# Kernel optimization log

Measured on AMD Instinct MI355X. Metric: run time of the kernel, lower is better.

## Reference

```python
import math
import jax, jax.numpy as jnp
from jax import lax
import numpy as np

LIDAR_MAX_X = 32.0
LIDAR_MAX_Y = 32.0
NQ = 1280  # eval-branch num_queries hardcoded in the torch module


def sineembed(pos, hidden_dim=256):
    # pos (..., 2) -> (..., hidden_dim); DAB-DETR sine embedding
    half = hidden_dim // 2
    dim_t = 10000.0 ** (2.0 * (jnp.arange(half) // 2).astype(jnp.float32) / half)
    scale = 2.0 * math.pi
    px = (pos[..., 0] * scale)[..., None] / dim_t
    py = (pos[..., 1] * scale)[..., None] / dim_t

    def interleave(p):
        s = jnp.stack([jnp.sin(p[..., 0::2]), jnp.cos(p[..., 1::2])], axis=-1)
        return s.reshape(s.shape[:-2] + (-1,))

    return jnp.concatenate([interleave(py), interleave(px)], axis=-1)


def grid_sample_bilinear_zeros(value, grid):
    # value (B,C,H,W); grid (B,Hg,Wg,2) in [-1,1], (x,y) order,
    # bilinear, padding_mode='zeros', align_corners=False
    B, C, H, W = value.shape
    Hg, Wg = grid.shape[1], grid.shape[2]
    gx = ((grid[..., 0] + 1.0) * 0.5 * W - 0.5).reshape(B, -1)
    gy = ((grid[..., 1] + 1.0) * 0.5 * H - 0.5).reshape(B, -1)
    x0 = jnp.floor(gx)
    y0 = jnp.floor(gy)
    wx1 = gx - x0
    wy1 = gy - y0
    vflat = value.reshape(B, C, H * W)

    def gather(ix, iy, w):
        valid = (ix >= 0) & (ix <= W - 1) & (iy >= 0) & (iy <= H - 1)
        ixc = jnp.clip(ix, 0, W - 1).astype(jnp.int32)
        iyc = jnp.clip(iy, 0, H - 1).astype(jnp.int32)
        idx = iyc * W + ixc  # (B,N)
        v = jnp.take_along_axis(vflat, idx[:, None, :], axis=2)  # (B,C,N)
        return v * (w * valid)[:, None, :]

    out = (gather(x0, y0, (1 - wx1) * (1 - wy1))
           + gather(x0 + 1, y0, wx1 * (1 - wy1))
           + gather(x0, y0 + 1, (1 - wx1) * wy1)
           + gather(x0 + 1, y0 + 1, wx1 * wy1))
    return out.reshape(B, C, Hg, Wg)


def setup_inputs() -> dict:
    key = jax.random.key(0)
    ks = jax.random.split(key, 12)
    B, D, Cin, H, W = 8, 256, 64, 200, 200
    return {
        "queries": jax.random.normal(ks[0], (B, NQ, D), jnp.float32),
        "navi_points": jax.random.normal(ks[1], (B, 2), jnp.float32) * 10.0,
        "bev_feature": jax.random.normal(ks[2], (B, Cin, H, W), jnp.float32),
        "spatial_shape": jnp.array([H, W], jnp.int32),
        "point_score": jax.random.uniform(ks[3], (B, 2), jnp.float32),
        "aw_w": jax.random.normal(ks[4], (1, D), jnp.float32) * 0.02,
        "aw_b": jnp.zeros((1,), jnp.float32),
        "aws_w": jax.random.normal(ks[5], (1, D), jnp.float32) * 0.02,
        "aws_b": jnp.zeros((1,), jnp.float32),
        "conv_w": jax.random.normal(ks[6], (256, Cin, 3, 3), jnp.float32) * 0.02,
        "conv_b": jnp.zeros((256,), jnp.float32),
        "out_w": jax.random.normal(ks[7], (D, D), jnp.float32) * 0.02,
        "out_b": jnp.zeros((D,), jnp.float32),
    }


def reference(queries, navi_points, bev_feature, spatial_shape, point_score,
              aw_w, aw_b, aws_w, aws_b, conv_w, conv_b, out_w, out_b):
    B, nq, D = queries.shape
    # eval branch: expand navi_points to (B, 1280, 1, 2)
    pts = jnp.broadcast_to(navi_points.reshape(B, 1, 1, 2), (B, NQ, 1, 2))
    # normalize then swap -> grid (x=pts_y/max_x, y=pts_x/max_y)
    grid = jnp.stack([pts[..., 1] / LIDAR_MAX_X, pts[..., 0] / LIDAR_MAX_Y], axis=-1)

    # attention weights from queries, softmax over num_points (=1)
    aw = jax.nn.softmax(queries @ aw_w.T + aw_b, axis=-1)  # (B,NQ,1)

    # score weights from sine embedding of point_score
    ps = jnp.broadcast_to(point_score.reshape(B, 1, 1, 2), (B, NQ, 1, 2))
    aws = (sineembed(ps) @ aws_w.T + aws_b).reshape(B, NQ, 1)  # (B,NQ,1)

    # value projection: Conv2d 64->256, 3x3, pad 1, ReLU
    value = lax.conv_general_dilated(bev_feature, conv_w, (1, 1), 'SAME',
                                     dimension_numbers=('NCHW', 'OIHW', 'NCHW'))
    value = jax.nn.relu(value + conv_b[None, :, None, None])

    sampled = grid_sample_bilinear_zeros(value, grid)  # (B,256,NQ,1)

    out = (aw[:, None] * sampled * aws[:, None]).sum(axis=-1)  # (B,256,NQ)
    out = out.transpose(0, 2, 1)  # (B,NQ,256)
    out = out @ out_w.T + out_b
    return out + queries  # dropout is identity at inference
```

## Files before the change

kernel.cpp:

```cpp
#include <hip/hip_runtime.h>
#include <math.h>

#define NQ   1280
#define DD   256
#define CIN  64
#define HH   200
#define WW   200
#define KW   576

__device__ __forceinline__ float wave_reduce(float v) {
#pragma unroll
    for (int off = 32; off > 0; off >>= 1) v += __shfl_down(v, off, 64);
    return v;
}

__global__ __launch_bounds__(256) void conv_sample_kernel(
    const float* __restrict__ navi,
    const float* __restrict__ bev,
    const float* __restrict__ pscore,
    const float* __restrict__ aws_w,
    const float* __restrict__ aws_b,
    const float* __restrict__ conv_w,
    const float* __restrict__ conv_b,
    float* __restrict__ s_out,
    float* __restrict__ aws_out)
{
    const int b    = blockIdx.x >> 6;
    const int cg   = blockIdx.x & 63;
    const int tid  = threadIdx.x;
    const int lane = tid & 63;
    const int wave = tid >> 6;

    __shared__ float win[CIN][16];
    __shared__ float wv[4][KW];
    __shared__ float red[DD];

    float nx = navi[b * 2 + 0];
    float ny = navi[b * 2 + 1];
    float gx = (ny * (1.0f / 32.0f) + 1.0f) * 0.5f * (float)WW - 0.5f;
    float gy = (nx * (1.0f / 32.0f) + 1.0f) * 0.5f * (float)HH - 0.5f;
    float x0f = floorf(gx), y0f = floorf(gy);
    float wx1 = gx - x0f, wy1 = gy - y0f;
    int x0 = (int)x0f, y0 = (int)y0f;

    float cw[4];
    {
        float wx[2] = {1.0f - wx1, wx1};
        float wy[2] = {1.0f - wy1, wy1};
#pragma unroll
        for (int k = 0; k < 4; ++k) {
            int dx = k & 1, dy = k >> 1;
            float ixf = x0f + (float)dx, iyf = y0f + (float)dy;
            bool valid = (ixf >= 0.0f) && (ixf <= (float)(WW - 1)) &&
                         (iyf >= 0.0f) && (iyf <= (float)(HH - 1));
            cw[k] = wx[dx] * wy[dy] * (valid ? 1.0f : 0.0f);
        }
    }

    for (int idx = tid; idx < CIN * 16; idx += 256) {
        int ci = idx >> 4, pos = idx & 15;
        int yy = y0 - 1 + (pos >> 2);
        int xx = x0 - 1 + (pos & 3);
        float v = 0.0f;
        if (yy >= 0 && yy < HH && xx >= 0 && xx < WW)
            v = bev[((size_t)b * CIN + ci) * (HH * WW) + (size_t)yy * WW + xx];
        win[ci][pos] = v;
    }
    __syncthreads();

    for (int idx = tid; idx < 4 * KW; idx += 256) {
        int corner = idx / KW, k = idx - corner * KW;
        int ci = k / 9, r = k - ci * 9;
        int ky = r / 3, kx = r - ky * 3;
        int dy = corner >> 1, dx = corner & 1;
        wv[corner][k] = win[ci][(ky + dy) * 4 + (kx + dx)];
    }
    __syncthreads();

    const int c = cg * 4 + wave;
    const float* wp = conv_w + (size_t)c * KW;
    float a0 = 0.f, a1 = 0.f, a2 = 0.f, a3 = 0.f;
#pragma unroll
    for (int i = 0; i < 9; ++i) {
        float w = wp[i * 64 + lane];
        a0 = fmaf(w, wv[0][i * 64 + lane], a0);
        a1 = fmaf(w, wv[1][i * 64 + lane], a1);
        a2 = fmaf(w, wv[2][i * 64 + lane], a2);
        a3 = fmaf(w, wv[3][i * 64 + lane], a3);
    }
    a0 = wave_reduce(a0);
    a1 = wave_reduce(a1);
    a2 = wave_reduce(a2);
    a3 = wave_reduce(a3);
    if (lane == 0) {
        float cb = conv_b[c];
        float v0 = fmaxf(a0 + cb, 0.0f);
        float v1 = fmaxf(a1 + cb, 0.0f);
        float v2 = fmaxf(a2 + cb, 0.0f);
        float v3 = fmaxf(a3 + cb, 0.0f);
        s_out[b * DD + c] = cw[0] * v0 + cw[1] * v1 + cw[2] * v2 + cw[3] * v3;
    }

    if (cg == 0) {
        float psx = pscore[b * 2 + 0];
        float psy = pscore[b * 2 + 1];
        float p = (tid < 128) ? psy : psx;
        int j = (tid & 127) >> 1;
        float dimt = powf(10000.0f, (float)j * (1.0f / 64.0f));
        float arg = p * 6.283185307179586f / dimt;
        float e = (tid & 1) ? cosf(arg) : sinf(arg);
        red[tid] = e * aws_w[tid];
        __syncthreads();
        for (int off = 128; off > 0; off >>= 1) {
            if (tid < off) red[tid] += red[tid + off];
            __syncthreads();
        }
        if (tid == 0) aws_out[b] = red[0] + aws_b[0];
    }
}

__global__ __launch_bounds__(256) void matvec_kernel(
    const float* __restrict__ out_w,
    const float* __restrict__ out_b,
    const float* __restrict__ s_in,
    const float* __restrict__ aws_in,
    float* __restrict__ t_out)
{
    const int b    = blockIdx.x >> 6;
    const int cg   = blockIdx.x & 63;
    const int tid  = threadIdx.x;
    const int lane = tid & 63;
    const int wave = tid >> 6;

    __shared__ float s_sh[DD];
    s_sh[tid] = s_in[b * DD + tid];
    __syncthreads();

    const int d = cg * 4 + wave;
    const float* wp = out_w + (size_t)d * DD;
    float sum = 0.0f;
#pragma unroll
    for (int i = 0; i < 4; ++i)
        sum = fmaf(wp[i * 64 + lane], s_sh[i * 64 + lane], sum);
    sum = wave_reduce(sum);
    if (lane == 0) t_out[b * DD + d] = aws_in[b] * sum + out_b[d];
}

__global__ __launch_bounds__(256) void add_kernel(
    const float4* __restrict__ q4,
    const float4* __restrict__ t4,
    float4* __restrict__ out4,
    int total4)
{
    int i = blockIdx.x * blockDim.x + threadIdx.x;
    if (i >= total4) return;
    float4 v = q4[i];
    int d4 = i & (DD / 4 - 1);
    int b = i / (NQ * DD / 4);
    float4 tv = t4[b * (DD / 4) + d4];
    v.x += tv.x; v.y += tv.y; v.z += tv.z; v.w += tv.w;
    out4[i] = v;
}

extern "C" void kernel_launch(void* const* d_in, const int* in_sizes, int n_in,
                              void* d_out, int out_size, void* d_ws, size_t ws_size,
                              hipStream_t stream) {
    const float* queries = (const float*)d_in[0];
    const float* navi    = (const float*)d_in[1];
    const float* bev     = (const float*)d_in[2];
    const float* pscore  = (const float*)d_in[4];
    const float* aws_w   = (const float*)d_in[7];
    const float* aws_b   = (const float*)d_in[8];
    const float* conv_w  = (const float*)d_in[9];
    const float* conv_b  = (const float*)d_in[10];
    const float* out_w   = (const float*)d_in[11];
    const float* out_b   = (const float*)d_in[12];
    float* out = (float*)d_out;

    const int B = in_sizes[1] / 2;

    float* s   = (float*)d_ws;
    float* aws = s + B * DD;
    float* t   = s + B * DD + 256;

    conv_sample_kernel<<<B * 64, 256, 0, stream>>>(navi, bev, pscore, aws_w,
                                                   aws_b, conv_w, conv_b, s, aws);
    matvec_kernel<<<B * 64, 256, 0, stream>>>(out_w, out_b, s, aws, t);

    int total4 = B * NQ * DD / 4;
    add_kernel<<<(total4 + 255) / 256, 256, 0, stream>>>(
        (const float4*)queries, (const float4*)t, (float4*)out, total4);
}
```

Measured before the change: 145.6 us.

## Fuse conv-sample, matvec and residual add into one cooperative kernel

Replaces three kernel launches with a single cooperative launch of 512 blocks that uses grid-wide syncs between the conv/sample stage, the output projection matvec, and the residual add. The conv stage now indexes the shared 4x4 window directly instead of building a per-corner staging buffer, which drops one shared-memory pass and a barrier. The residual add is done by a fixed grid that loops over the output. This aims to remove launch overhead and inter-kernel gaps, at the cost of grid.sync latency and a fixed batch size hardcoded at compile time.

```diff
diff --git a/kernel.cpp b/kernel.cpp
--- a/kernel.cpp
+++ b/kernel.cpp
@@ -1,12 +1,20 @@
 #include <hip/hip_runtime.h>
+#include <hip/hip_cooperative_groups.h>
 #include <math.h>
+
+namespace cg = cooperative_groups;
 
 #define NQ   1280
 #define DD   256
 #define CIN  64
 #define HH   200
 #define WW   200
+#define BB   8
 #define KW   576
+#define GRID 512
+#define TPB  256
+#define NTH  (GRID * TPB)
+#define TOTAL4 (BB * NQ * DD / 4)
 
 __device__ __forceinline__ float wave_reduce(float v) {
 #pragma unroll
@@ -14,7 +22,7 @@
     return v;
 }
 
-__global__ __launch_bounds__(256) void conv_sample_kernel(
+__global__ __launch_bounds__(256) void fused_kernel(
     const float* __restrict__ navi,
     const float* __restrict__ bev,
     const float* __restrict__ pscore,
@@ -22,144 +30,139 @@
     const float* __restrict__ aws_b,
     const float* __restrict__ conv_w,
     const float* __restrict__ conv_b,
-    float* __restrict__ s_out,
-    float* __restrict__ aws_out)
+    const float* __restrict__ out_w,
+    const float* __restrict__ out_b,
+    const float4* __restrict__ q4,
+    float4* __restrict__ out4,
+    float* __restrict__ s_g,
+    float* __restrict__ aws_g,
+    float* __restrict__ t_g)
 {
+    cg::grid_group grid = cg::this_grid();
     const int b    = blockIdx.x >> 6;
-    const int cg   = blockIdx.x & 63;
+    const int cgp  = blockIdx.x & 63;
     const int tid  = threadIdx.x;
     const int lane = tid & 63;
     const int wave = tid >> 6;
 
-    __shared__ float win[CIN][16];
-    __shared__ float wv[4][KW];
+    __shared__ float win[CIN * 16];
     __shared__ float red[DD];
 
-    float nx = navi[b * 2 + 0];
-    float ny = navi[b * 2 + 1];
-    float gx = (ny * (1.0f / 32.0f) + 1.0f) * 0.5f * (float)WW - 0.5f;
-    float gy = (nx * (1.0f / 32.0f) + 1.0f) * 0.5f * (float)HH - 0.5f;
-    float x0f = floorf(gx), y0f = floorf(gy);
-    float wx1 = gx - x0f, wy1 = gy - y0f;
-    int x0 = (int)x0f, y0 = (int)y0f;
+    {
+        float nx = navi[b * 2 + 0];
+        float ny = navi[b * 2 + 1];
+        float gx = (ny * (1.0f / 32.0f) + 1.0f) * 0.5f * (float)WW - 0.5f;
+        float gy = (nx * (1.0f / 32.0f) + 1.0f) * 0.5f * (float)HH - 0.5f;
+        float x0f = floorf(gx), y0f = floorf(gy);
+        float wx1 = gx - x0f, wy1 = gy - y0f;
+        int x0 = (int)x0f, y0 = (int)y0f;
 
-    float cw[4];
-    {
-        float wx[2] = {1.0f - wx1, wx1};
-        float wy[2] = {1.0f - wy1, wy1};
+        float cw[4];
+        {
+            float wx[2] = {1.0f - wx1, wx1};
+            float wy[2] = {1.0f - wy1, wy1};
 #pragma unroll
-        for (int k = 0; k < 4; ++k) {
-            int dx = k & 1, dy = k >> 1;
-            float ixf = x0f + (float)dx, iyf = y0f + (float)dy;
-            bool valid = (ixf >= 0.0f) && (ixf <= (float)(WW - 1)) &&
-                         (iyf >= 0.0f) && (iyf <= (float)(HH - 1));
-            cw[k] = wx[dx] * wy[dy] * (valid ? 1.0f : 0.0f);
+            for (int k = 0; k < 4; ++k) {
+                int dx = k & 1, dy = k >> 1;
+                float ixf = x0f + (float)dx, iyf = y0f + (float)dy;
+                bool valid = (ixf >= 0.0f) && (ixf <= (float)(WW - 1)) &&
+                             (iyf >= 0.0f) && (iyf <= (float)(HH - 1));
+                cw[k] = wx[dx] * wy[dy] * (valid ? 1.0f : 0.0f);
+            }
+        }
+
+        for (int idx = tid; idx < CIN * 16; idx += TPB) {
+            int ci = idx >> 4, pos = idx & 15;
+            int yy = y0 - 1 + (pos >> 2);
+            int xx = x0 - 1 + (pos & 3);
+            float v = 0.0f;
+            if (yy >= 0 && yy < HH && xx >= 0 && xx < WW)
+                v = bev[((size_t)b * CIN + ci) * (HH * WW) + (size_t)yy * WW + xx];
+            win[idx] = v;
+        }
+        __syncthreads();
+
+        const int c = cgp * 4 + wave;
+        const float* wp = conv_w + (size_t)c * KW;
+        float a0 = 0.f, a1 = 0.f, a2 = 0.f, a3 = 0.f;
+#pragma unroll
+        for (int i = 0; i < 9; ++i) {
+            int k  = i * 64 + lane;
+            int ci = k / 9;
+            int r  = k - ci * 9;
+            int ky = r / 3;
+            int kx = r - ky * 3;
+            int base = ci * 16 + ky * 4 + kx;
+            float w = wp[k];
+            a0 = fmaf(w, win[base],     a0);
+            a1 = fmaf(w, win[base + 1], a1);
+            a2 = fmaf(w, win[base + 4], a2);
+            a3 = fmaf(w, win[base + 5], a3);
+        }
+        a0 = wave_reduce(a0);
+        a1 = wave_reduce(a1);
+        a2 = wave_reduce(a2);
+        a3 = wave_reduce(a3);
+        if (lane == 0) {
+            float cb = conv_b[c];
+            float v0 = fmaxf(a0 + cb, 0.0f);
+            float v1 = fmaxf(a1 + cb, 0.0f);
+            float v2 = fmaxf(a2 + cb, 0.0f);
+            float v3 = fmaxf(a3 + cb, 0.0f);
+            s_g[b * DD + c] = cw[0] * v0 + cw[1] * v1 + cw[2] * v2 + cw[3] * v3;
+        }
+
+        if (cgp == 0) {
+            float psx = pscore[b * 2 + 0];
+            float psy = pscore[b * 2 + 1];
+            float p = (tid < 128) ? psy : psx;
+            int j = (tid & 127) >> 1;
+            float dimt = powf(10000.0f, (float)j * (1.0f / 64.0f));
+            float arg = p * 6.283185307179586f / dimt;
+            float e = (tid & 1) ? cosf(arg) : sinf(arg);
+            red[tid] = e * aws_w[tid];
+            __syncthreads();
+            for (int off = 128; off > 0; off >>= 1) {
+                if (tid < off) red[tid] += red[tid + off];
+                __syncthreads();
+            }
+            if (tid == 0) aws_g[b] = red[0] + aws_b[0];
         }
     }
 
-    for (int idx = tid; idx < CIN * 16; idx += 256) {
-        int ci = idx >> 4, pos = idx & 15;
-        int yy = y0 - 1 + (pos >> 2);
-        int xx = x0 - 1 + (pos & 3);
-        float v = 0.0f;
-        if (yy >= 0 && yy < HH && xx >= 0 && xx < WW)
-            v = bev[((size_t)b * CIN + ci) * (HH * WW) + (size_t)yy * WW + xx];
-        win[ci][pos] = v;
-    }
-    __syncthreads();
+    __threadfence();
+    grid.sync();
 
-    for (int idx = tid; idx < 4 * KW; idx += 256) {
-        int corner = idx / KW, k = idx - corner * KW;
-        int ci = k / 9, r = k - ci * 9;
-        int ky = r / 3, kx = r - ky * 3;
-        int dy = corner >> 1, dx = corner & 1;
-        wv[corner][k] = win[ci][(ky + dy) * 4 + (kx + dx)];
-    }
-    __syncthreads();
-
-    const int c = cg * 4 + wave;
-    const float* wp = conv_w + (size_t)c * KW;
-    float a0 = 0.f, a1 = 0.f, a2 = 0.f, a3 = 0.f;
+    {
+        red[tid] = s_g[b * DD + tid];
+        __syncthreads();
+        const int d = cgp * 4 + wave;
+        const float* wp = out_w + (size_t)d * DD;
+        float sum = 0.0f;
 #pragma unroll
-    for (int i = 0; i < 9; ++i) {
-        float w = wp[i * 64 + lane];
-        a0 = fmaf(w, wv[0][i * 64 + lane], a0);
-        a1 = fmaf(w, wv[1][i * 64 + lane], a1);
-        a2 = fmaf(w, wv[2][i * 64 + lane], a2);
-        a3 = fmaf(w, wv[3][i * 64 + lane], a3);
-    }
-    a0 = wave_reduce(a0);
-    a1 = wave_reduce(a1);
-    a2 = wave_reduce(a2);
-    a3 = wave_reduce(a3);
-    if (lane == 0) {
-        float cb = conv_b[c];
-        float v0 = fmaxf(a0 + cb, 0.0f);
-        float v1 = fmaxf(a1 + cb, 0.0f);
-        float v2 = fmaxf(a2 + cb, 0.0f);
-        float v3 = fmaxf(a3 + cb, 0.0f);
-        s_out[b * DD + c] = cw[0] * v0 + cw[1] * v1 + cw[2] * v2 + cw[3] * v3;
+        for (int i = 0; i < 4; ++i)
+            sum = fmaf(wp[i * 64 + lane], red[i * 64 + lane], sum);
+        sum = wave_reduce(sum);
+        if (lane == 0) t_g[b * DD + d] = aws_g[b] * sum + out_b[d];
     }
 
-    if (cg == 0) {
-        float psx = pscore[b * 2 + 0];
-        float psy = pscore[b * 2 + 1];
-        float p = (tid < 128) ? psy : psx;
-        int j = (tid & 127) >> 1;
-        float dimt = powf(10000.0f, (float)j * (1.0f / 64.0f));
-        float arg = p * 6.283185307179586f / dimt;
-        float e = (tid & 1) ? cosf(arg) : sinf(arg);
-        red[tid] = e * aws_w[tid];
-        __syncthreads();
-        for (int off = 128; off > 0; off >>= 1) {
-            if (tid < off) red[tid] += red[tid + off];
-            __syncthreads();
+    __threadfence();
+    grid.sync();
+
+    {
+        const float4* t4 = (const float4*)t_g;
+        const int base = blockIdx.x * TPB + tid;
+#pragma unroll
+        for (int k = 0; k < TOTAL4 / NTH; ++k) {
+            int i = base + k * NTH;
+            float4 v = q4[i];
+            int bb = i / (NQ * DD / 4);
+            int d4 = i & (DD / 4 - 1);
+            float4 tv = t4[bb * (DD / 4) + d4];
+            v.x += tv.x; v.y += tv.y; v.z += tv.z; v.w += tv.w;
+            out4[i] = v;
         }
-        if (tid == 0) aws_out[b] = red[0] + aws_b[0];
     }
-}
-
-__global__ __launch_bounds__(256) void matvec_kernel(
-    const float* __restrict__ out_w,
-    const float* __restrict__ out_b,
-    const float* __restrict__ s_in,
-    const float* __restrict__ aws_in,
-    float* __restrict__ t_out)
-{
-    const int b    = blockIdx.x >> 6;
-    const int cg   = blockIdx.x & 63;
-    const int tid  = threadIdx.x;
-    const int lane = tid & 63;
-    const int wave = tid >> 6;
-
-    __shared__ float s_sh[DD];
-    s_sh[tid] = s_in[b * DD + tid];
-    __syncthreads();
-
-    const int d = cg * 4 + wave;
-    const float* wp = out_w + (size_t)d * DD;
-    float sum = 0.0f;
-#pragma unroll
-    for (int i = 0; i < 4; ++i)
-        sum = fmaf(wp[i * 64 + lane], s_sh[i * 64 + lane], sum);
-    sum = wave_reduce(sum);
-    if (lane == 0) t_out[b * DD + d] = aws_in[b] * sum + out_b[d];
-}
-
-__global__ __launch_bounds__(256) void add_kernel(
-    const float4* __restrict__ q4,
-    const float4* __restrict__ t4,
-    float4* __restrict__ out4,
-    int total4)
-{
-    int i = blockIdx.x * blockDim.x + threadIdx.x;
-    if (i >= total4) return;
-    float4 v = q4[i];
-    int d4 = i & (DD / 4 - 1);
-    int b = i / (NQ * DD / 4);
-    float4 tv = t4[b * (DD / 4) + d4];
-    v.x += tv.x; v.y += tv.y; v.z += tv.z; v.w += tv.w;
-    out4[i] = v;
 }
 
 extern "C" void kernel_launch(void* const* d_in, const int* in_sizes, int n_in,
@@ -175,19 +178,17 @@
     const float* conv_b  = (const float*)d_in[10];
     const float* out_w   = (const float*)d_in[11];
     const float* out_b   = (const float*)d_in[12];
-    float* out = (float*)d_out;
-
-    const int B = in_sizes[1] / 2;
+    const float4* q4 = (const float4*)queries;
+    float4* out4 = (float4*)d_out;
 
     float* s   = (float*)d_ws;
-    float* aws = s + B * DD;
-    float* t   = s + B * DD + 256;
+    float* aws = s + BB * DD;
+    float* t   = s + BB * DD + 256;
 
-    conv_sample_kernel<<<B * 64, 256, 0, stream>>>(navi, bev, pscore, aws_w,
-                                                   aws_b, conv_w, conv_b, s, aws);
-    matvec_kernel<<<B * 64, 256, 0, stream>>>(out_w, out_b, s, aws, t);
-
-    int total4 = B * NQ * DD / 4;
-    add_kernel<<<(total4 + 255) / 256, 256, 0, stream>>>(
-        (const float4*)queries, (const float4*)t, (float4*)out, total4);
+    void* args[] = {
+        (void*)&navi, (void*)&bev, (void*)&pscore, (void*)&aws_w, (void*)&aws_b,
+        (void*)&conv_w, (void*)&conv_b, (void*)&out_w, (void*)&out_b,
+        (void*)&q4, (void*)&out4, (void*)&s, (void*)&aws, (void*)&t};
+    hipLaunchCooperativeKernel((void*)fused_kernel, dim3(GRID), dim3(TPB),
+                               args, 0, stream);
 }
```

Measured after the change: 352.6 us. 142% more time.
